# Kernel optimization log

Measured on AMD Instinct MI355X. Metric: run time of the kernel, lower is better.

The kernel has to match this reference:

```python
import jax, jax.numpy as jnp
import numpy as np

B, S, H, I, E, K = 4, 2048, 1024, 4096, 8, 2


def setup_inputs() -> dict:
    key = jax.random.key(0)
    k1, k2, k3, k4, k5, k6 = jax.random.split(key, 6)
    hidden_states = jax.random.normal(k1, (B, S, H), dtype=jnp.float32)
    routing_weights = jax.random.uniform(k2, (B, S, K), dtype=jnp.float32)
    selected_experts = jax.random.randint(k3, (B, S, K), 0, E, dtype=jnp.int32)
    std = 0.02
    W_in = jax.random.normal(k4, (E, H, I), dtype=jnp.float32) * std
    W_v = jax.random.normal(k5, (E, H, I), dtype=jnp.float32) * std
    W_out = jax.random.normal(k6, (E, I, H), dtype=jnp.float32) * std
    return {
        "hidden_states": hidden_states,
        "routing_weights": routing_weights,
        "selected_experts": selected_experts,
        "W_in": W_in,
        "W_v": W_v,
        "W_out": W_out,
    }


def reference(hidden_states, routing_weights, selected_experts, W_in, W_v, W_out):
    # Faithful naive MoE: every expert's gated MLP is run on ALL tokens,
    # then masked by (selected_experts == e) * routing_weights and summed.
    n_experts = W_in.shape[0]
    final = jnp.zeros_like(hidden_states)
    for e in range(n_experts):  # fixed small structural loop over experts
        gated = jax.nn.gelu(hidden_states @ W_in[e]) * (hidden_states @ W_v[e])  # [B,S,I]
        expert_out = gated @ W_out[e]  # [B,S,H]
        # weight per token: sum over top_k slots matching this expert -> [B,S,1]
        w = jnp.sum(jnp.where(selected_experts == e, routing_weights, 0.0), axis=-1)[:, :, None]
        final = final + w * expert_out
    return final
```

## Files before the change

kernel.cpp:

```cpp
#include <hip/hip_runtime.h>
#include <hip/hip_bf16.h>

typedef unsigned short u16;
typedef __attribute__((ext_vector_type(8))) short short8;
typedef __attribute__((ext_vector_type(4))) float f32x4;
typedef __attribute__((ext_vector_type(4))) u16 u16x4;
typedef __attribute__((ext_vector_type(8))) u16 u16x8;

#define T_TOK 8192
#define NSLOT 16384
#define H_DIM 1024
#define I_DIM 4096
#define N_EXP 8
#define MAXTILES 144

#define O_META 0
#define O_ETOK 4096
#define O_EW   (O_ETOK + NSLOT * 4)
#define O_XB   (256 * 1024)
#define O_WIN  (O_XB + (size_t)T_TOK * H_DIM * 2)
#define O_WV   (O_WIN + (size_t)N_EXP * I_DIM * H_DIM * 2)
#define O_WOUT (O_WV + (size_t)N_EXP * I_DIM * H_DIM * 2)
#define O_G    (O_WOUT + (size_t)N_EXP * H_DIM * I_DIM * 2)


__device__ __forceinline__ u16 f2bf(float f) {
  union { float f; unsigned u; } v; v.f = f;
  unsigned r = v.u + 0x7FFFu + ((v.u >> 16) & 1u);
  return (u16)(r >> 16);
}

#define GLL(g, l) __builtin_amdgcn_global_load_lds( \
    (const __attribute__((address_space(1))) void*)(g), \
    (__attribute__((address_space(3))) void*)(l), 16, 0, 0)

#define MFMA16(a, b, c) __builtin_amdgcn_mfma_f32_16x16x32_bf16(a, b, c, 0, 0, 0)

__global__ void route_count(const int* __restrict__ sel, int* __restrict__ meta) {
  __shared__ int cnt[N_EXP];
  const int tid = threadIdx.x;
  if (tid < N_EXP) cnt[tid] = 0;
  __syncthreads();
  for (int i = tid; i < NSLOT; i += 256) atomicAdd(&cnt[sel[i]], 1);
  __syncthreads();
  if (tid == 0) {
    int run = 0, tc = 0;
    for (int e = 0; e < N_EXP; ++e) {
      const int c = cnt[e];
      meta[448 + e] = run;
      const int nt = (c + 127) >> 7;
      for (int t = 0; t < nt; ++t) {
        meta[16 + tc] = e;
        meta[160 + tc] = run + t * 128;
        int end = run + t * 128 + 128;
        if (end > run + c) end = run + c;
        meta[304 + tc] = end;
        ++tc;
      }
      run += c;
    }
    meta[0] = tc;
  }
}

__global__ void route_fill(const int* __restrict__ sel, const float* __restrict__ rw,
                           int* __restrict__ meta, int* __restrict__ etok,
                           float* __restrict__ ew) {
  const int i = blockIdx.x * 256 + threadIdx.x;
  if (i >= NSLOT) return;
  const int e = sel[i];
  const int pos = atomicAdd(&meta[448 + e], 1);
  etok[pos] = i >> 1;
  ew[pos] = rw[i];
}

__global__ void conv_x(const float* __restrict__ x, u16* __restrict__ xb) {
  const size_t i = ((size_t)blockIdx.x * 256 + threadIdx.x) * 4;
  const float4 v = *(const float4*)&x[i];
  u16x4 o;
  o.x = f2bf(v.x); o.y = f2bf(v.y); o.z = f2bf(v.z); o.w = f2bf(v.w);
  *(u16x4*)&xb[i] = o;
}

__global__ void transp_conv(const float* __restrict__ src, u16* __restrict__ dst,
                            int R, int C) {
  __shared__ float t[64][65];
  const int tid = threadIdx.x;
  const int mat = blockIdx.z;
  const int rb = blockIdx.y * 64, cb = blockIdx.x * 64;
  const float* s = src + (size_t)mat * R * C + (size_t)rb * C + cb;
#pragma unroll
  for (int it = 0; it < 4; ++it) {
    const int r = it * 16 + (tid >> 4);
    const int c = (tid & 15) * 4;
    const float4 v = *(const float4*)&s[(size_t)r * C + c];
    t[r][c] = v.x; t[r][c + 1] = v.y; t[r][c + 2] = v.z; t[r][c + 3] = v.w;
  }
  __syncthreads();
  u16* d = dst + (size_t)mat * R * C + (size_t)cb * R + rb;
#pragma unroll
  for (int it = 0; it < 2; ++it) {
    const int oc = it * 32 + (tid >> 3);
    const int j0 = (tid & 7) * 8;
    u16x8 o;
#pragma unroll
    for (int j = 0; j < 8; ++j) o[j] = f2bf(t[j0 + j][oc]);
    *(u16x8*)&d[(size_t)oc * R + j0] = o;
  }
}

__global__ __launch_bounds__(256) void gemm1(
    const u16* __restrict__ Xb, const u16* __restrict__ Wi,
    const u16* __restrict__ Wv, u16* __restrict__ Gout,
    const int* __restrict__ meta, const int* __restrict__ etok) {
  const int tile = blockIdx.y;
  if (tile >= meta[0]) return;
  const int e  = meta[16 + tile];
  const int r0 = meta[160 + tile];
  const int r1 = meta[304 + tile];
  const int n0 = blockIdx.x << 7;

  __shared__ __align__(16) u16 As[2][4096];
  __shared__ __align__(16) u16 Bi[2][4096];
  __shared__ __align__(16) u16 Bv[2][4096];

  const int tid = threadIdx.x;
  const int t0 = tid, t1 = tid + 256;
  const int rA0 = t0 >> 2, rA1 = t1 >> 2;
  const int sc0 = ((t0 & 3) ^ (rA0 & 3)) << 3;
  const int sc1 = ((t1 & 3) ^ (rA1 & 3)) << 3;
  int ia0 = r0 + rA0; if (ia0 >= r1) ia0 = r0;
  int ia1 = r0 + rA1; if (ia1 >= r1) ia1 = r0;
  const u16* gA0 = Xb + (size_t)etok[ia0] * H_DIM + sc0;
  const u16* gA1 = Xb + (size_t)etok[ia1] * H_DIM + sc1;
  const size_t wb = ((size_t)e * I_DIM + n0) * H_DIM;
  const u16* gBi0 = Wi + wb + (size_t)rA0 * H_DIM + sc0;
  const u16* gBi1 = Wi + wb + (size_t)rA1 * H_DIM + sc1;
  const u16* gBv0 = Wv + wb + (size_t)rA0 * H_DIM + sc0;
  const u16* gBv1 = Wv + wb + (size_t)rA1 * H_DIM + sc1;

  const int lane = tid & 63;
  const int wid = tid >> 6;
  const int wm = (wid >> 1) << 6, wn = (wid & 1) << 6;
  const int lr = lane & 15, q = lane >> 4;
  const int cq = (q ^ (lr & 3)) << 3;
  int aoff[4], boff[4];
#pragma unroll
  for (int i = 0; i < 4; ++i) {
    aoff[i] = (wm + i * 16 + lr) * 32 + cq;
    boff[i] = (wn + i * 16 + lr) * 32 + cq;
  }

  f32x4 ci[4][4], cv[4][4];
#pragma unroll
  for (int i = 0; i < 4; ++i)
#pragma unroll
    for (int j = 0; j < 4; ++j) { ci[i][j] = (f32x4)0.0f; cv[i][j] = (f32x4)0.0f; }

#define STAGE1(b, kt) do { const int ko = (kt) << 5;                      \
    GLL(gA0 + ko, &As[b][t0 * 8]);  GLL(gA1 + ko, &As[b][t1 * 8]);        \
    GLL(gBi0 + ko, &Bi[b][t0 * 8]); GLL(gBi1 + ko, &Bi[b][t1 * 8]);       \
    GLL(gBv0 + ko, &Bv[b][t0 * 8]); GLL(gBv1 + ko, &Bv[b][t1 * 8]); } while (0)

  STAGE1(0, 0);
  __syncthreads();
  int buf = 0;
  for (int kt = 0; kt < H_DIM / 32; ++kt) {
    if (kt + 1 < H_DIM / 32) STAGE1(buf ^ 1, kt + 1);
    short8 a[4], fi[4], fv[4];
#pragma unroll
    for (int i = 0; i < 4; ++i) a[i] = *(const short8*)&As[buf][aoff[i]];
#pragma unroll
    for (int j = 0; j < 4; ++j) fi[j] = *(const short8*)&Bi[buf][boff[j]];
#pragma unroll
    for (int j = 0; j < 4; ++j) fv[j] = *(const short8*)&Bv[buf][boff[j]];
#pragma unroll
    for (int i = 0; i < 4; ++i)
#pragma unroll
      for (int j = 0; j < 4; ++j) {
        ci[i][j] = MFMA16(a[i], fi[j], ci[i][j]);
        cv[i][j] = MFMA16(a[i], fv[j], cv[i][j]);
      }
    __syncthreads();
    buf ^= 1;
  }

  u16* gbase = Gout + (size_t)tile * 128 * I_DIM;
#pragma unroll
  for (int i = 0; i < 4; ++i)
#pragma unroll
    for (int t = 0; t < 4; ++t) {
      const int row = wm + i * 16 + q * 4 + t;
      u16* grow = gbase + (size_t)row * I_DIM + n0 + wn + lr;
#pragma unroll
      for (int j = 0; j < 4; ++j) {
        const float x = ci[i][j][t];
        const float g = 0.5f * x *
            (1.0f + tanhf(0.7978845608f * (x + 0.044715f * x * x * x)));
        grow[j * 16] = f2bf(g * cv[i][j][t]);
      }
    }
}

__global__ __launch_bounds__(256) void gemm2(
    const u16* __restrict__ Gin, const u16* __restrict__ Wo,
    float* __restrict__ out, const int* __restrict__ meta,
    const int* __restrict__ etok, const float* __restrict__ ew) {
  const int tile = blockIdx.y;
  if (tile >= meta[0]) return;
  const int e  = meta[16 + tile];
  const int r0 = meta[160 + tile];
  const int r1 = meta[304 + tile];
  const int n0 = blockIdx.x << 7;

  __shared__ __align__(16) u16 As[2][4096];
  __shared__ __align__(16) u16 Bs[2][4096];
  __shared__ int tok_s[128];
  __shared__ float w_s[128];

  const int tid = threadIdx.x;
  if (tid < 128) {
    const int idx = r0 + tid;
    const bool v = idx < r1;
    tok_s[tid] = v ? etok[idx] : -1;
    w_s[tid] = v ? ew[idx] : 0.0f;
  }

  const int t0 = tid, t1 = tid + 256;
  const int rA0 = t0 >> 2, rA1 = t1 >> 2;
  const int sc0 = ((t0 & 3) ^ (rA0 & 3)) << 3;
  const int sc1 = ((t1 & 3) ^ (rA1 & 3)) << 3;
  const u16* gA0 = Gin + ((size_t)tile * 128 + rA0) * I_DIM + sc0;
  const u16* gA1 = Gin + ((size_t)tile * 128 + rA1) * I_DIM + sc1;
  const size_t wb = (size_t)e * H_DIM * I_DIM;
  const u16* gB0 = Wo + wb + (size_t)(n0 + rA0) * I_DIM + sc0;
  const u16* gB1 = Wo + wb + (size_t)(n0 + rA1) * I_DIM + sc1;

  const int lane = tid & 63;
  const int wid = tid >> 6;
  const int wm = (wid >> 1) << 6, wn = (wid & 1) << 6;
  const int lr = lane & 15, q = lane >> 4;
  const int cq = (q ^ (lr & 3)) << 3;
  int aoff[4], boff[4];
#pragma unroll
  for (int i = 0; i < 4; ++i) {
    aoff[i] = (wm + i * 16 + lr) * 32 + cq;
    boff[i] = (wn + i * 16 + lr) * 32 + cq;
  }

  f32x4 c[4][4];
#pragma unroll
  for (int i = 0; i < 4; ++i)
#pragma unroll
    for (int j = 0; j < 4; ++j) c[i][j] = (f32x4)0.0f;

#define STAGE2(b, kt) do { const int ko = (kt) << 5;                  \
    GLL(gA0 + ko, &As[b][t0 * 8]); GLL(gA1 + ko, &As[b][t1 * 8]);     \
    GLL(gB0 + ko, &Bs[b][t0 * 8]); GLL(gB1 + ko, &Bs[b][t1 * 8]); } while (0)

  STAGE2(0, 0);
  __syncthreads();
  int buf = 0;
  for (int kt = 0; kt < I_DIM / 32; ++kt) {
    if (kt + 1 < I_DIM / 32) STAGE2(buf ^ 1, kt + 1);
    short8 a[4], b_[4];
#pragma unroll
    for (int i = 0; i < 4; ++i) a[i] = *(const short8*)&As[buf][aoff[i]];
#pragma unroll
    for (int j = 0; j < 4; ++j) b_[j] = *(const short8*)&Bs[buf][boff[j]];
#pragma unroll
    for (int i = 0; i < 4; ++i)
#pragma unroll
      for (int j = 0; j < 4; ++j) c[i][j] = MFMA16(a[i], b_[j], c[i][j]);
    __syncthreads();
    buf ^= 1;
  }

#pragma unroll
  for (int i = 0; i < 4; ++i)
#pragma unroll
    for (int t = 0; t < 4; ++t) {
      const int row = wm + i * 16 + q * 4 + t;
      const int tk = tok_s[row];
      if (tk >= 0) {
        const float wgt = w_s[row];
        float* orow = out + (size_t)tk * H_DIM + n0 + wn + lr;
#pragma unroll
        for (int j = 0; j < 4; ++j) atomicAdd(&orow[j * 16], wgt * c[i][j][t]);
      }
    }
}

extern "C" void kernel_launch(void* const* d_in, const int* in_sizes, int n_in,
                              void* d_out, int out_size, void* d_ws, size_t ws_size,
                              hipStream_t stream) {
  const float* hs   = (const float*)d_in[0];
  const float* rw   = (const float*)d_in[1];
  const int*   sel  = (const int*)d_in[2];
  const float* w_in = (const float*)d_in[3];
  const float* w_v  = (const float*)d_in[4];
  const float* w_out = (const float*)d_in[5];
  float* out = (float*)d_out;
  char* ws = (char*)d_ws;
  int* meta  = (int*)(ws + O_META);
  int* etok  = (int*)(ws + O_ETOK);
  float* ew  = (float*)(ws + O_EW);
  u16* xb = (u16*)(ws + O_XB);
  u16* wi = (u16*)(ws + O_WIN);
  u16* wv = (u16*)(ws + O_WV);
  u16* wo = (u16*)(ws + O_WOUT);
  u16* g  = (u16*)(ws + O_G);

  hipMemsetAsync(out, 0, (size_t)T_TOK * H_DIM * sizeof(float), stream);
  route_count<<<1, 256, 0, stream>>>(sel, meta);
  route_fill<<<NSLOT / 256, 256, 0, stream>>>(sel, rw, meta, etok, ew);
  conv_x<<<(T_TOK * H_DIM / 4) / 256, 256, 0, stream>>>(hs, xb);
  transp_conv<<<dim3(I_DIM / 64, H_DIM / 64, N_EXP), 256, 0, stream>>>(w_in, wi, H_DIM, I_DIM);
  transp_conv<<<dim3(I_DIM / 64, H_DIM / 64, N_EXP), 256, 0, stream>>>(w_v, wv, H_DIM, I_DIM);
  transp_conv<<<dim3(H_DIM / 64, I_DIM / 64, N_EXP), 256, 0, stream>>>(w_out, wo, I_DIM, H_DIM);
  gemm1<<<dim3(I_DIM / 128, MAXTILES), 256, 0, stream>>>(xb, wi, wv, g, meta, etok);
  gemm2<<<dim3(H_DIM / 128, MAXTILES), 256, 0, stream>>>(g, wo, out, meta, etok, ew);
}
```

Measured before the change: 1.347 ms.

## Interleave W_in/W_v into one matrix and replace atomic scatter with combine pass

The gate and value weights are transposed into a single interleaved matrix in 16-column blocks, so gemm1 runs one 128x128 tile with a single B operand and pairs gate/value accumulators in its epilogue. This halves per-block accumulator and LDS use but doubles the grid. Gemm2 now writes per-slot outputs densely instead of using float atomicAdd into the output. A new combine kernel uses an inverse slot map to sum the two weighted expert outputs per token, which also removes the output memset. The tanh in GELU is now computed with __expf, and the slot-output buffer reuses the concatenated-weight workspace region, which is safe only because gemm1 has already consumed it.

```diff
diff --git a/kernel.cpp b/kernel.cpp
--- a/kernel.cpp
+++ b/kernel.cpp
@@ -11,17 +11,19 @@
 #define NSLOT 16384
 #define H_DIM 1024
 #define I_DIM 4096
+#define N_CAT 8192
 #define N_EXP 8
 #define MAXTILES 144
 
 #define O_META 0
 #define O_ETOK 4096
 #define O_EW   (O_ETOK + NSLOT * 4)
+#define O_INV  (O_EW + NSLOT * 4)
 #define O_XB   (256 * 1024)
-#define O_WIN  (O_XB + (size_t)T_TOK * H_DIM * 2)
-#define O_WV   (O_WIN + (size_t)N_EXP * I_DIM * H_DIM * 2)
-#define O_WOUT (O_WV + (size_t)N_EXP * I_DIM * H_DIM * 2)
-#define O_G    (O_WOUT + (size_t)N_EXP * H_DIM * I_DIM * 2)
+#define O_WCAT (O_XB + (size_t)T_TOK * H_DIM * 2)
+#define O_WOUT (O_WCAT + (size_t)N_EXP * N_CAT * H_DIM * 2)
+#define O_G    (O_WOUT + (size_t)N_EXP * I_DIM * H_DIM * 2)
+#define O_OS   O_WCAT
 
 
 __device__ __forceinline__ u16 f2bf(float f) {
@@ -65,13 +67,14 @@
 
 __global__ void route_fill(const int* __restrict__ sel, const float* __restrict__ rw,
                            int* __restrict__ meta, int* __restrict__ etok,
-                           float* __restrict__ ew) {
+                           float* __restrict__ ew, int* __restrict__ inv) {
   const int i = blockIdx.x * 256 + threadIdx.x;
   if (i >= NSLOT) return;
   const int e = sel[i];
   const int pos = atomicAdd(&meta[448 + e], 1);
   etok[pos] = i >> 1;
   ew[pos] = rw[i];
+  inv[i] = pos;
 }
 
 __global__ void conv_x(const float* __restrict__ x, u16* __restrict__ xb) {
@@ -83,7 +86,7 @@
 }
 
 __global__ void transp_conv(const float* __restrict__ src, u16* __restrict__ dst,
-                            int R, int C) {
+                            int R, int C, int mode) {
   __shared__ float t[64][65];
   const int tid = threadIdx.x;
   const int mat = blockIdx.z;
@@ -97,22 +100,25 @@
     t[r][c] = v.x; t[r][c + 1] = v.y; t[r][c + 2] = v.z; t[r][c + 3] = v.w;
   }
   __syncthreads();
-  u16* d = dst + (size_t)mat * R * C + (size_t)cb * R + rb;
+  const size_t dstride = (mode == 2) ? (size_t)R * C : 2 * (size_t)R * C;
+  u16* dd = dst + (size_t)mat * dstride;
 #pragma unroll
   for (int it = 0; it < 2; ++it) {
-    const int oc = it * 32 + (tid >> 3);
+    const int ocl = it * 32 + (tid >> 3);
+    const int oc = cb + ocl;
+    const int mrow = (mode == 2) ? oc : (((oc >> 4) << 5) | (mode << 4) | (oc & 15));
     const int j0 = (tid & 7) * 8;
     u16x8 o;
 #pragma unroll
-    for (int j = 0; j < 8; ++j) o[j] = f2bf(t[j0 + j][oc]);
-    *(u16x8*)&d[(size_t)oc * R + j0] = o;
+    for (int j = 0; j < 8; ++j) o[j] = f2bf(t[j0 + j][oc - cb]);
+    *(u16x8*)&dd[(size_t)mrow * R + rb + j0] = o;
   }
 }
 
 __global__ __launch_bounds__(256) void gemm1(
-    const u16* __restrict__ Xb, const u16* __restrict__ Wi,
-    const u16* __restrict__ Wv, u16* __restrict__ Gout,
-    const int* __restrict__ meta, const int* __restrict__ etok) {
+    const u16* __restrict__ Xb, const u16* __restrict__ Wc,
+    u16* __restrict__ Gout, const int* __restrict__ meta,
+    const int* __restrict__ etok) {
   const int tile = blockIdx.y;
   if (tile >= meta[0]) return;
   const int e  = meta[16 + tile];
@@ -121,8 +127,7 @@
   const int n0 = blockIdx.x << 7;
 
   __shared__ __align__(16) u16 As[2][4096];
-  __shared__ __align__(16) u16 Bi[2][4096];
-  __shared__ __align__(16) u16 Bv[2][4096];
+  __shared__ __align__(16) u16 Bs[2][4096];
 
   const int tid = threadIdx.x;
   const int t0 = tid, t1 = tid + 256;
@@ -133,11 +138,8 @@
   int ia1 = r0 + rA1; if (ia1 >= r1) ia1 = r0;
   const u16* gA0 = Xb + (size_t)etok[ia0] * H_DIM + sc0;
   const u16* gA1 = Xb + (size_t)etok[ia1] * H_DIM + sc1;
-  const size_t wb = ((size_t)e * I_DIM + n0) * H_DIM;
-  const u16* gBi0 = Wi + wb + (size_t)rA0 * H_DIM + sc0;
-  const u16* gBi1 = Wi + wb + (size_t)rA1 * H_DIM + sc1;
-  const u16* gBv0 = Wv + wb + (size_t)rA0 * H_DIM + sc0;
-  const u16* gBv1 = Wv + wb + (size_t)rA1 * H_DIM + sc1;
+  const u16* gB0 = Wc + ((size_t)e * N_CAT + n0 + rA0) * H_DIM + sc0;
+  const u16* gB1 = Wc + ((size_t)e * N_CAT + n0 + rA1) * H_DIM + sc1;
 
   const int lane = tid & 63;
   const int wid = tid >> 6;
@@ -151,61 +153,57 @@
     boff[i] = (wn + i * 16 + lr) * 32 + cq;
   }
 
-  f32x4 ci[4][4], cv[4][4];
+  f32x4 c[4][4];
 #pragma unroll
   for (int i = 0; i < 4; ++i)
 #pragma unroll
-    for (int j = 0; j < 4; ++j) { ci[i][j] = (f32x4)0.0f; cv[i][j] = (f32x4)0.0f; }
-
-#define STAGE1(b, kt) do { const int ko = (kt) << 5;                      \
-    GLL(gA0 + ko, &As[b][t0 * 8]);  GLL(gA1 + ko, &As[b][t1 * 8]);        \
-    GLL(gBi0 + ko, &Bi[b][t0 * 8]); GLL(gBi1 + ko, &Bi[b][t1 * 8]);       \
-    GLL(gBv0 + ko, &Bv[b][t0 * 8]); GLL(gBv1 + ko, &Bv[b][t1 * 8]); } while (0)
+    for (int j = 0; j < 4; ++j) c[i][j] = (f32x4)0.0f;
+
+#define STAGE1(b, kt) do { const int ko = (kt) << 5;                  \
+    GLL(gA0 + ko, &As[b][t0 * 8]); GLL(gA1 + ko, &As[b][t1 * 8]);     \
+    GLL(gB0 + ko, &Bs[b][t0 * 8]); GLL(gB1 + ko, &Bs[b][t1 * 8]); } while (0)
 
   STAGE1(0, 0);
   __syncthreads();
   int buf = 0;
   for (int kt = 0; kt < H_DIM / 32; ++kt) {
     if (kt + 1 < H_DIM / 32) STAGE1(buf ^ 1, kt + 1);
-    short8 a[4], fi[4], fv[4];
+    short8 a[4], b_[4];
 #pragma unroll
     for (int i = 0; i < 4; ++i) a[i] = *(const short8*)&As[buf][aoff[i]];
 #pragma unroll
-    for (int j = 0; j < 4; ++j) fi[j] = *(const short8*)&Bi[buf][boff[j]];
-#pragma unroll
-    for (int j = 0; j < 4; ++j) fv[j] = *(const short8*)&Bv[buf][boff[j]];
+    for (int j = 0; j < 4; ++j) b_[j] = *(const short8*)&Bs[buf][boff[j]];
 #pragma unroll
     for (int i = 0; i < 4; ++i)
 #pragma unroll
-      for (int j = 0; j < 4; ++j) {
-        ci[i][j] = MFMA16(a[i], fi[j], ci[i][j]);
-        cv[i][j] = MFMA16(a[i], fv[j], cv[i][j]);
-      }
+      for (int j = 0; j < 4; ++j) c[i][j] = MFMA16(a[i], b_[j], c[i][j]);
     __syncthreads();
     buf ^= 1;
   }
 
-  u16* gbase = Gout + (size_t)tile * 128 * I_DIM;
+  u16* gb = Gout + (size_t)tile * 128 * I_DIM;
+  const int gcb = (n0 + wn) >> 1;
 #pragma unroll
   for (int i = 0; i < 4; ++i)
 #pragma unroll
     for (int t = 0; t < 4; ++t) {
       const int row = wm + i * 16 + q * 4 + t;
-      u16* grow = gbase + (size_t)row * I_DIM + n0 + wn + lr;
-#pragma unroll
-      for (int j = 0; j < 4; ++j) {
-        const float x = ci[i][j][t];
-        const float g = 0.5f * x *
-            (1.0f + tanhf(0.7978845608f * (x + 0.044715f * x * x * x)));
-        grow[j * 16] = f2bf(g * cv[i][j][t]);
+      u16* grow = gb + (size_t)row * I_DIM + gcb + lr;
+#pragma unroll
+      for (int p = 0; p < 2; ++p) {
+        const float x = c[i][2 * p][t];
+        const float v = c[i][2 * p + 1][t];
+        const float u = 0.7978845608f * (x + 0.044715f * x * x * x);
+        const float texp = __expf(2.0f * u);
+        const float th = 1.0f - 2.0f / (texp + 1.0f);
+        grow[p * 16] = f2bf(0.5f * x * (1.0f + th) * v);
       }
     }
 }
 
 __global__ __launch_bounds__(256) void gemm2(
     const u16* __restrict__ Gin, const u16* __restrict__ Wo,
-    float* __restrict__ out, const int* __restrict__ meta,
-    const int* __restrict__ etok, const float* __restrict__ ew) {
+    float* __restrict__ Os, const int* __restrict__ meta) {
   const int tile = blockIdx.y;
   if (tile >= meta[0]) return;
   const int e  = meta[16 + tile];
@@ -215,17 +213,8 @@
 
   __shared__ __align__(16) u16 As[2][4096];
   __shared__ __align__(16) u16 Bs[2][4096];
-  __shared__ int tok_s[128];
-  __shared__ float w_s[128];
 
   const int tid = threadIdx.x;
-  if (tid < 128) {
-    const int idx = r0 + tid;
-    const bool v = idx < r1;
-    tok_s[tid] = v ? etok[idx] : -1;
-    w_s[tid] = v ? ew[idx] : 0.0f;
-  }
-
   const int t0 = tid, t1 = tid + 256;
   const int rA0 = t0 >> 2, rA1 = t1 >> 2;
   const int sc0 = ((t0 & 3) ^ (rA0 & 3)) << 3;
@@ -281,43 +270,59 @@
 #pragma unroll
     for (int t = 0; t < 4; ++t) {
       const int row = wm + i * 16 + q * 4 + t;
-      const int tk = tok_s[row];
-      if (tk >= 0) {
-        const float wgt = w_s[row];
-        float* orow = out + (size_t)tk * H_DIM + n0 + wn + lr;
-#pragma unroll
-        for (int j = 0; j < 4; ++j) atomicAdd(&orow[j * 16], wgt * c[i][j][t]);
+      const int gp = r0 + row;
+      if (gp < r1) {
+        float* orow = Os + (size_t)gp * H_DIM + n0 + wn + lr;
+#pragma unroll
+        for (int j = 0; j < 4; ++j) orow[j * 16] = c[i][j][t];
       }
     }
+}
+
+__global__ void combine(const float* __restrict__ Os, const int* __restrict__ inv,
+                        const float* __restrict__ ew, float* __restrict__ out) {
+  const int t = blockIdx.x;
+  const int c4 = threadIdx.x * 4;
+  const int p0 = inv[2 * t], p1 = inv[2 * t + 1];
+  const float w0 = ew[p0], w1 = ew[p1];
+  const float4 a = *(const float4*)&Os[(size_t)p0 * H_DIM + c4];
+  const float4 b = *(const float4*)&Os[(size_t)p1 * H_DIM + c4];
+  float4 o;
+  o.x = w0 * a.x + w1 * b.x;
+  o.y = w0 * a.y + w1 * b.y;
+  o.z = w0 * a.z + w1 * b.z;
+  o.w = w0 * a.w + w1 * b.w;
+  *(float4*)&out[(size_t)t * H_DIM + c4] = o;
 }
 
 extern "C" void kernel_launch(void* const* d_in, const int* in_sizes, int n_in,
                               void* d_out, int out_size, void* d_ws, size_t ws_size,
                               hipStream_t stream) {
-  const float* hs   = (const float*)d_in[0];
-  const float* rw   = (const float*)d_in[1];
-  const int*   sel  = (const int*)d_in[2];
-  const float* w_in = (const float*)d_in[3];
-  const float* w_v  = (const float*)d_in[4];
+  const float* hs    = (const float*)d_in[0];
+  const float* rw    = (const float*)d_in[1];
+  const int*   sel   = (const int*)d_in[2];
+  const float* w_in  = (const float*)d_in[3];
+  const float* w_v   = (const float*)d_in[4];
   const float* w_out = (const float*)d_in[5];
   float* out = (float*)d_out;
   char* ws = (char*)d_ws;
-  int* meta  = (int*)(ws + O_META);
-  int* etok  = (int*)(ws + O_ETOK);
-  float* ew  = (float*)(ws + O_EW);
-  u16* xb = (u16*)(ws + O_XB);
-  u16* wi = (u16*)(ws + O_WIN);
-  u16* wv = (u16*)(ws + O_WV);
-  u16* wo = (u16*)(ws + O_WOUT);
-  u16* g  = (u16*)(ws + O_G);
-
-  hipMemsetAsync(out, 0, (size_t)T_TOK * H_DIM * sizeof(float), stream);
+  int* meta   = (int*)(ws + O_META);
+  int* etok   = (int*)(ws + O_ETOK);
+  float* ew   = (float*)(ws + O_EW);
+  int* inv    = (int*)(ws + O_INV);
+  u16* xb     = (u16*)(ws + O_XB);
+  u16* wcat   = (u16*)(ws + O_WCAT);
+  u16* wo     = (u16*)(ws + O_WOUT);
+  u16* g      = (u16*)(ws + O_G);
+  float* os   = (float*)(ws + O_OS);
+
   route_count<<<1, 256, 0, stream>>>(sel, meta);
-  route_fill<<<NSLOT / 256, 256, 0, stream>>>(sel, rw, meta, etok, ew);
+  route_fill<<<NSLOT / 256, 256, 0, stream>>>(sel, rw, meta, etok, ew, inv);
   conv_x<<<(T_TOK * H_DIM / 4) / 256, 256, 0, stream>>>(hs, xb);
-  transp_conv<<<dim3(I_DIM / 64, H_DIM / 64, N_EXP), 256, 0, stream>>>(w_in, wi, H_DIM, I_DIM);
-  transp_conv<<<dim3(I_DIM / 64, H_DIM / 64, N_EXP), 256, 0, stream>>>(w_v, wv, H_DIM, I_DIM);
-  transp_conv<<<dim3(H_DIM / 64, I_DIM / 64, N_EXP), 256, 0, stream>>>(w_out, wo, I_DIM, H_DIM);
-  gemm1<<<dim3(I_DIM / 128, MAXTILES), 256, 0, stream>>>(xb, wi, wv, g, meta, etok);
-  gemm2<<<dim3(H_DIM / 128, MAXTILES), 256, 0, stream>>>(g, wo, out, meta, etok, ew);
-}
+  transp_conv<<<dim3(I_DIM / 64, H_DIM / 64, N_EXP), 256, 0, stream>>>(w_in, wcat, H_DIM, I_DIM, 0);
+  transp_conv<<<dim3(I_DIM / 64, H_DIM / 64, N_EXP), 256, 0, stream>>>(w_v, wcat, H_DIM, I_DIM, 1);
+  transp_conv<<<dim3(H_DIM / 64, I_DIM / 64, N_EXP), 256, 0, stream>>>(w_out, wo, I_DIM, H_DIM, 2);
+  gemm1<<<dim3(N_CAT / 128, MAXTILES), 256, 0, stream>>>(xb, wcat, g, meta, etok);
+  gemm2<<<dim3(H_DIM / 128, MAXTILES), 256, 0, stream>>>(g, wo, os, meta);
+  combine<<<T_TOK, 256, 0, stream>>>(os, inv, ew, out);
+}
```

Measured after the change: 1.176 ms. -12.7%, faster.
